# Performance work log

Hardware: AMD Instinct MI355X
Metric: run time of the kernel (lower is better)

## Reference

```python
import jax, jax.numpy as jnp
import numpy as np

# static sinkhorn parameters (match SamplesLoss init kwargs)
P = 2
BLUR = 0.05
SCALING = 0.5
DIAMETER = 2.0  # points on the unit sphere => diameter <= 2

# geomloss epsilon_schedule: [diameter^p] + exp(arange(p*log(d), p*log(blur), p*log(scaling))) + [blur^p]
EPS_LIST = (
    [DIAMETER ** P]
    + [float(np.exp(e)) for e in np.arange(P * np.log(DIAMETER), P * np.log(BLUR), P * np.log(SCALING))]
    + [BLUR ** P]
)


def cost(m, n):
    # spherical (geodesic) distance / 2 between unit vectors: acos(<m,n>)/2
    t = jnp.clip(jnp.einsum('bnd,bmd->bnm', m, n), -1.0 + 1e-6, 1.0 - 1e-6)
    return jnp.arccos(t) * 0.5  # (B,N,M)


def softmin(eps, C, wlog):
    # -eps * logsumexp(wlog[B,1,M] - C/eps, axis=2) -> (B,N)
    return -eps * jax.nn.logsumexp(wlog[:, None, :] - C / eps, axis=2)


def log_weights(a):
    return jnp.where(a > 0, jnp.log(jnp.maximum(a, 1e-30)), -1e5)


def setup_inputs() -> dict:
    key = jax.random.key(0)
    kx, ky = jax.random.split(key)
    B, N, M, D = 8, 2048, 2048, 3
    x = jax.random.normal(kx, (B, N, D), dtype=jnp.float32)
    y = jax.random.normal(ky, (B, M, D), dtype=jnp.float32)
    # project onto the unit sphere (spherical cost assumes unit vectors)
    x = x / jnp.linalg.norm(x, axis=-1, keepdims=True)
    y = y / jnp.linalg.norm(y, axis=-1, keepdims=True)
    alpha = jnp.ones((B, N), dtype=jnp.float32) / N
    beta = jnp.ones((B, M), dtype=jnp.float32) / M
    return {"alpha": alpha, "x": x, "beta": beta, "y": y}


def reference(alpha, x, beta, y):
    sg = jax.lax.stop_gradient
    # second argument of each cost is detached, as in the torch code
    C_xx = cost(x, sg(x))
    C_yy = cost(y, sg(y))
    C_xy = cost(x, sg(y))
    C_yx = cost(y, sg(x))
    al = log_weights(alpha)
    bl = log_weights(beta)

    # ---- sinkhorn loop (torch.no_grad section) ----
    Cxx_, Cyy_, Cxy_, Cyx_, al_, bl_ = map(sg, (C_xx, C_yy, C_xy, C_yx, al, bl))
    eps = EPS_LIST[0]
    a_x = softmin(eps, Cxx_, al_)   # OT(a,a) potential on x
    b_y = softmin(eps, Cyy_, bl_)   # OT(b,b) potential on y
    a_y = softmin(eps, Cyx_, al_)   # OT(a,b) potential on y
    b_x = softmin(eps, Cxy_, bl_)   # OT(a,b) potential on x
    for eps in EPS_LIST:  # annealed, symmetrized sinkhorn updates
        at_x = softmin(eps, Cxx_, al_ + a_x / eps)
        bt_y = softmin(eps, Cyy_, bl_ + b_y / eps)
        at_y = softmin(eps, Cyx_, al_ + b_x / eps)
        bt_x = softmin(eps, Cxy_, bl_ + a_y / eps)
        a_x, b_y = 0.5 * (a_x + at_x), 0.5 * (b_y + bt_y)
        a_y, b_x = 0.5 * (a_y + at_y), 0.5 * (b_x + bt_x)

    # ---- last extrapolation, differentiable (eps = blur^p) ----
    eps = EPS_LIST[-1]
    a_x = softmin(eps, C_xx, sg(al + a_x / eps))
    b_y = softmin(eps, C_yy, sg(bl + b_y / eps))
    a_y = softmin(eps, C_yx, sg(al + b_x / eps))
    b_x = softmin(eps, C_xy, sg(bl + a_y / eps))

    # balanced (reach=None), debiased sinkhorn cost -> (B,)
    return jnp.sum(alpha * (b_x - a_x), axis=-1) + jnp.sum(beta * (a_y - b_y), axis=-1)
```

## Files before the change

### kernel.cpp

```cpp
#include <hip/hip_runtime.h>
#include <math.h>

#define BB 8
#define NN 2048
#define L2E 1.4426950408889634f
#define LN2 0.6931471805599453f
#define PI_F 3.14159265358979f
#define CLIP 0.999999f
#define THSC 20860.0f
#define THSCI (1.0f / 20860.0f)

constexpr int TB   = 128;
constexpr int T16  = NN / TB;
constexpr int NXX  = T16 * (T16 + 1) / 2;
constexpr int NT   = 2 * NXX + T16 * T16;
constexpr int SARR = BB * NN;

__device__ __forceinline__ void decode_tile(int bx, int& kind, int& I, int& J) {
    if (bx < NXX) kind = 0;
    else if (bx < 2 * NXX) { kind = 1; bx -= NXX; }
    else { kind = 2; bx -= 2 * NXX; }
    if (kind < 2) {
        int idx = bx; I = 0;
        for (;;) { int len = T16 - I; if (idx < len) { J = I + idx; break; } idx -= len; I++; }
    } else { I = bx >> 4; J = bx & 15; }
}

__device__ __forceinline__ float acos_raw(float d) {
    const float u = fabsf(d);
    float pl = fmaf(u, -0.0187293f, 0.0742610f);
    pl = fmaf(u, pl, -0.2121144f); pl = fmaf(u, pl, 1.5707288f);
    const float rt = __builtin_amdgcn_sqrtf(1.f - u) * pl;
    return (d >= 0.f) ? rt : (PI_F - rt);
}

__device__ __forceinline__ size_t th_off(int g, int wv, int lane) {
    return (size_t)(((g * 4 + wv) * 64 + lane) * 8);
}

__global__ __launch_bounds__(256)
void pack_kernel(const float* __restrict__ alpha, const float* __restrict__ beta,
                 float* __restrict__ gxw, float* __restrict__ gyw,
                 float* __restrict__ Wall, float* __restrict__ Gall)
{
    const int tid = threadIdx.x;
    const int gid = blockIdx.x * 256 + tid;
    const int o = gid >> 14, i = gid & (SARR - 1);
    const float* w = (o == 0 || o == 3) ? alpha : beta;
    const float v = w[i];
    const float g = ((v > 0.f) ? logf(fmaxf(v, 1e-30f)) : -1e5f) * L2E;
    if (o == 0) gxw[i] = g;
    if (o == 1) gyw[i] = g;
    float m = g;
    m = fmaxf(m, __shfl_xor(m, 1));  m = fmaxf(m, __shfl_xor(m, 2));
    m = fmaxf(m, __shfl_xor(m, 4));  m = fmaxf(m, __shfl_xor(m, 8));
    m = fmaxf(m, __shfl_xor(m, 16)); m = fmaxf(m, __shfl_xor(m, 32));
    __shared__ float wmax[4];
    const int wv = tid >> 6;
    if ((tid & 63) == 0) wmax[wv] = m;
    __syncthreads();
    const int grp = tid >> 7;
    const float G = fmaxf(wmax[grp * 2], wmax[grp * 2 + 1]);
    Wall[gid] = __builtin_amdgcn_exp2f(g - G);
    if ((tid & 127) == 0) Gall[gid >> 7] = G;
}

__global__ __launch_bounds__(256)
void maxes_kernel(const float* __restrict__ x, const float* __restrict__ y,
                  float* __restrict__ Rxx, float* __restrict__ Ryy,
                  float* __restrict__ Rxy, float* __restrict__ Cxy,
                  unsigned short* __restrict__ Theta,
                  const float* __restrict__ Wall, const float* __restrict__ Gall,
                  float2* pAX, float2* pBY, float2* pAY, float2* pBX,
                  float negK, int writeTheta)
{
    __shared__ float4 p1s[TB], p2s[TB];
    __shared__ float colred[4][TB];
    __shared__ float colpart[4][TB];
    int kind, I, J; decode_tile(blockIdx.x, kind, I, J);
    const int b = blockIdx.y, t = threadIdx.x;
    const float* P1 = (kind == 1) ? y : x;
    const float* P2 = (kind == 0) ? x : y;
    const int o1 = (kind == 0) ? 0 : (kind == 1) ? 1 : 3;
    const int o2 = (kind == 0) ? 0 : (kind == 1) ? 1 : 2;
    float2* rowOut = (kind == 0) ? pAX : (kind == 1) ? pBY : pBX;
    float2* colOut = (kind == 0) ? pAX : (kind == 1) ? pBY : pAY;
    const bool diag = (kind < 2) && (I == J);
    const float* W1 = Wall + (size_t)o1 * SARR;
    const float* W2 = Wall + (size_t)o2 * SARR;

    if (t < TB) {
        size_t gi = (size_t)b * NN + (size_t)I * TB + t;
        p1s[t] = make_float4(P1[gi * 3], P1[gi * 3 + 1], P1[gi * 3 + 2], W1[gi]);
    } else {
        int u = t - TB; size_t gi = (size_t)b * NN + (size_t)J * TB + u;
        p2s[u] = make_float4(P2[gi * 3], P2[gi * 3 + 1], P2[gi * 3 + 2], W2[gi]);
    }
    const float G1 = Gall[o1 * 128 + b * T16 + I];
    const float G2 = Gall[o2 * 128 + b * T16 + J];
    __syncthreads();
    const int lane = t & 63, wv = t >> 6, colg = lane & 7, rowg = lane >> 3;
    const int r0 = wv * 32 + rowg * 4;
    unsigned short* Tb = Theta + ((size_t)(b * NT + blockIdx.x) << 14);

    float4 pr[4];
#pragma unroll
    for (int rr = 0; rr < 4; rr++) pr[rr] = p1s[r0 + rr];
    float rmx[4] = {-2.f, -2.f, -2.f, -2.f};
    float cmx[16];
#pragma unroll
    for (int j = 0; j < 16; j++) cmx[j] = -2.f;
    float racc[4] = {0.f, 0.f, 0.f, 0.f};
    float cacc[16];
#pragma unroll
    for (int j = 0; j < 16; j++) cacc[j] = 0.f;

#pragma unroll
    for (int g = 0; g < 8; g++) {
        uint4 outv;
#pragma unroll
        for (int e = 0; e < 2; e++) {
            const int j = g * 2 + e;
            const float4 q = p2s[colg + 8 * j];
            unsigned int lo = 0, hi = 0;
#pragma unroll
            for (int rr = 0; rr < 4; rr++) {
                const float d = fmaf(pr[rr].x, q.x, fmaf(pr[rr].y, q.y, pr[rr].z * q.z));
                rmx[rr] = fmaxf(rmx[rr], d);
                cmx[j] = fmaxf(cmx[j], d);
                if (writeTheta) {
                    const float dc = fminf(fmaxf(d, -CLIP), CLIP);
                    const float th = acos_raw(dc);
                    const unsigned int qv = __float2uint_rn(th * THSC);
                    if (rr == 0) lo = qv;
                    else if (rr == 1) lo |= qv << 16;
                    else if (rr == 2) hi = qv;
                    else hi |= qv << 16;
                    const float em = __builtin_amdgcn_exp2f(th * negK);
                    racc[rr] = fmaf(q.w, em, racc[rr]);
                    cacc[j]  = fmaf(pr[rr].w, em, cacc[j]);
                }
            }
            if (e == 0) { outv.x = lo; outv.y = hi; }
            else        { outv.z = lo; outv.w = hi; }
        }
        if (writeTheta)
            *(uint4*)(Tb + th_off(g, wv, lane)) = outv;
    }

#pragma unroll
    for (int rr = 0; rr < 4; rr++) {
        float v = rmx[rr];
        v = fmaxf(v, __shfl_xor(v, 1)); v = fmaxf(v, __shfl_xor(v, 2));
        v = fmaxf(v, __shfl_xor(v, 4));
        rmx[rr] = v;
    }
    if (colg == 0) {
        float* R = (kind == 0) ? Rxx : (kind == 1) ? Ryy : Rxy;
        const size_t base = ((size_t)b * T16 + J) * NN + (size_t)I * TB + r0;
#pragma unroll
        for (int rr = 0; rr < 4; rr++)
            R[base + rr] = acos_raw(fminf(fmaxf(rmx[rr], -CLIP), CLIP));
    }
#pragma unroll
    for (int j = 0; j < 16; j++) {
        float v = cmx[j];
        v = fmaxf(v, __shfl_xor(v, 8)); v = fmaxf(v, __shfl_xor(v, 16));
        v = fmaxf(v, __shfl_xor(v, 32));
        cmx[j] = v;
    }
    if (rowg == 0) {
#pragma unroll
        for (int j = 0; j < 16; j++) colred[wv][colg + 8 * j] = cmx[j];
    }

    if (writeTheta) {
#pragma unroll
        for (int j = 0; j < 16; j++) {
            float v = cacc[j];
            v += __shfl_xor(v, 8); v += __shfl_xor(v, 16); v += __shfl_xor(v, 32);
            cacc[j] = v;
        }
        if (rowg == 0) {
#pragma unroll
            for (int j = 0; j < 16; j++) colpart[wv][colg + 8 * j] = cacc[j];
        }
#pragma unroll
        for (int rr = 0; rr < 4; rr++) {
            float v = racc[rr];
            v += __shfl_xor(v, 1); v += __shfl_xor(v, 2); v += __shfl_xor(v, 4);
            racc[rr] = v;
        }
        if (colg == 0) {
            const size_t gr = (size_t)J * SARR + (size_t)b * NN + (size_t)I * TB + r0;
#pragma unroll
            for (int rr = 0; rr < 4; rr++)
                rowOut[gr + rr] = make_float2(G2, racc[rr]);
        }
    }

    __syncthreads();
    if (t < TB) {
        const float v = fmaxf(fmaxf(colred[0][t], colred[1][t]),
                              fmaxf(colred[2][t], colred[3][t]));
        const float th = acos_raw(fminf(fmaxf(v, -CLIP), CLIP));
        if (kind == 2) {
            Cxy[((size_t)b * T16 + I) * NN + (size_t)J * TB + t] = th;
        } else if (I != J) {
            float* R = (kind == 0) ? Rxx : Ryy;
            R[((size_t)b * T16 + I) * NN + (size_t)J * TB + t] = th;
        }
        if (writeTheta && !diag) {
            const float pv = colpart[0][t] + colpart[1][t] + colpart[2][t] + colpart[3][t];
            const size_t gc = (size_t)I * SARR + (size_t)b * NN + (size_t)J * TB + t;
            colOut[gc] = make_float2(G1, pv);
        }
    }
}

struct TileArgsT {
    const unsigned short* Theta;
    const float* Wall; const float* Gall;
    const float* Rxx; const float* Ryy; const float* Rxy; const float* Cxy;
    float2* pAX; float2* pBY; float2* pAY; float2* pBX;
};

__global__ __launch_bounds__(256)
void tile_theta_kernel(TileArgsT A, float ieh, float Kq)
{
    __shared__ float2 s1[TB], s2[TB];
    __shared__ float colpart[4][TB];
    int kind, I, J; decode_tile(blockIdx.x, kind, I, J);
    const int b = blockIdx.y, t = threadIdx.x;
    const int o1 = (kind == 0) ? 0 : (kind == 1) ? 1 : 3;
    const int o2 = (kind == 0) ? 0 : (kind == 1) ? 1 : 2;
    float2* rowOut = (kind == 0) ? A.pAX : (kind == 1) ? A.pBY : A.pBX;
    float2* colOut = (kind == 0) ? A.pAX : (kind == 1) ? A.pBY : A.pAY;
    const bool diag = (kind < 2) && (I == J);
    const float* W1 = A.Wall + (size_t)o1 * SARR;
    const float* W2 = A.Wall + (size_t)o2 * SARR;
    const float* Rrow = (kind == 0) ? A.Rxx : (kind == 1) ? A.Ryy : A.Rxy;
    const float* Csrc = (kind == 0) ? A.Rxx : (kind == 1) ? A.Ryy : A.Cxy;

    if (t < TB) {
        size_t gi = (size_t)b * NN + (size_t)I * TB + t;
        s1[t] = make_float2(Rrow[((size_t)b * T16 + J) * NN + (size_t)I * TB + t] * ieh, W1[gi]);
    } else {
        int u = t - TB; size_t gi = (size_t)b * NN + (size_t)J * TB + u;
        s2[u] = make_float2(Csrc[((size_t)b * T16 + I) * NN + (size_t)J * TB + u] * ieh, W2[gi]);
    }
    const float G1 = A.Gall[o1 * 128 + b * T16 + I];
    const float G2 = A.Gall[o2 * 128 + b * T16 + J];
    __syncthreads();

    const int lane = t & 63, wv = t >> 6, colg = lane & 7, rowg = lane >> 3;
    const int r0 = wv * 32 + rowg * 4;
    const unsigned short* Tb = A.Theta + ((size_t)(b * NT + blockIdx.x) << 14);

    float srr[4], w1r[4];
#pragma unroll
    for (int rr = 0; rr < 4; rr++) { const float2 v = s1[r0 + rr]; srr[rr] = v.x; w1r[rr] = v.y; }
    float racc[4] = {0.f, 0.f, 0.f, 0.f};
    float cacc[16];
#pragma unroll
    for (int j = 0; j < 16; j++) cacc[j] = 0.f;

#pragma unroll
    for (int g = 0; g < 8; g++) {
        const uint4 tq = *(const uint4*)(Tb + th_off(g, wv, lane));
#pragma unroll
        for (int e = 0; e < 2; e++) {
            const int j = g * 2 + e;
            const unsigned int lo = e ? tq.z : tq.x;
            const unsigned int hi = e ? tq.w : tq.y;
            const float2 sv = s2[colg + 8 * j];
            const float thv[4] = {
                (float)(lo & 0xffffu), (float)(lo >> 16),
                (float)(hi & 0xffffu), (float)(hi >> 16)
            };
#pragma unroll
            for (int rr = 0; rr < 4; rr++) {
                const float er = __builtin_amdgcn_exp2f(fmaf(thv[rr], -Kq, srr[rr]));
                const float ec = __builtin_amdgcn_exp2f(fmaf(thv[rr], -Kq, sv.x));
                racc[rr] = fmaf(sv.y, er, racc[rr]);
                cacc[j]  = fmaf(w1r[rr], ec, cacc[j]);
            }
        }
    }

#pragma unroll
    for (int j = 0; j < 16; j++) {
        float v = cacc[j];
        v += __shfl_xor(v, 8); v += __shfl_xor(v, 16); v += __shfl_xor(v, 32);
        cacc[j] = v;
    }
    if (rowg == 0) {
#pragma unroll
        for (int j = 0; j < 16; j++) colpart[wv][colg + 8 * j] = cacc[j];
    }
#pragma unroll
    for (int rr = 0; rr < 4; rr++) {
        float v = racc[rr];
        v += __shfl_xor(v, 1); v += __shfl_xor(v, 2); v += __shfl_xor(v, 4);
        racc[rr] = v;
    }
    if (colg == 0) {
        const size_t gr = (size_t)J * SARR + (size_t)b * NN + (size_t)I * TB + r0;
#pragma unroll
        for (int rr = 0; rr < 4; rr++)
            rowOut[gr + rr] = make_float2(G2 - srr[rr], racc[rr]);
    }
    __syncthreads();
    if (!diag && t < TB) {
        const float v = colpart[0][t] + colpart[1][t] + colpart[2][t] + colpart[3][t];
        const size_t gc = (size_t)I * SARR + (size_t)b * NN + (size_t)J * TB + t;
        colOut[gc] = make_float2(G1 - s2[t].x, v);
    }
}

struct TileArgs {
    const float* x; const float* y;
    const float* Wall; const float* Gall;
    const float* Rxx; const float* Ryy; const float* Rxy; const float* Cxy;
    float2* pAX; float2* pBY; float2* pAY; float2* pBX;
};

__global__ __launch_bounds__(256)
void tile_kernel(TileArgs A, float ieh, float pi_ieh)
{
    __shared__ float4 p1s[TB], p2s[TB];
    __shared__ float srs[TB], scs[TB];
    __shared__ float colpart[4][TB];
    int kind, I, J; decode_tile(blockIdx.x, kind, I, J);
    const int b = blockIdx.y, t = threadIdx.x;
    const float* P1 = (kind == 1) ? A.y : A.x;
    const float* P2 = (kind == 0) ? A.x : A.y;
    const int o1 = (kind == 0) ? 0 : (kind == 1) ? 1 : 3;
    const int o2 = (kind == 0) ? 0 : (kind == 1) ? 1 : 2;
    float2* rowOut = (kind == 0) ? A.pAX : (kind == 1) ? A.pBY : A.pBX;
    float2* colOut = (kind == 0) ? A.pAX : (kind == 1) ? A.pBY : A.pAY;
    const bool diag = (kind < 2) && (I == J);
    const float* W1 = A.Wall + (size_t)o1 * SARR;
    const float* W2 = A.Wall + (size_t)o2 * SARR;
    const float* Rrow = (kind == 0) ? A.Rxx : (kind == 1) ? A.Ryy : A.Rxy;
    const float* Csrc = (kind == 0) ? A.Rxx : (kind == 1) ? A.Ryy : A.Cxy;

    const float K0 = 1.5707288f * ieh, K1 = -0.2121144f * ieh;
    const float K2 = 0.0742610f * ieh, K3 = -0.0187293f * ieh;

    if (t < TB) {
        size_t gi = (size_t)b * NN + (size_t)I * TB + t;
        p1s[t] = make_float4(P1[gi * 3], P1[gi * 3 + 1], P1[gi * 3 + 2], W1[gi]);
        srs[t] = Rrow[((size_t)b * T16 + J) * NN + (size_t)I * TB + t] * ieh;
    } else {
        int u = t - TB; size_t gi = (size_t)b * NN + (size_t)J * TB + u;
        p2s[u] = make_float4(P2[gi * 3], P2[gi * 3 + 1], P2[gi * 3 + 2], W2[gi]);
        scs[u] = Csrc[((size_t)b * T16 + I) * NN + (size_t)J * TB + u] * ieh;
    }
    const float G1 = A.Gall[o1 * 128 + b * T16 + I];
    const float G2 = A.Gall[o2 * 128 + b * T16 + J];
    __syncthreads();

    const int lane = t & 63, wv = t >> 6, colg = lane & 7, rowg = lane >> 3;
    const int r0 = wv * 32 + rowg * 4;
    float4 pr[4]; float srr[4];
#pragma unroll
    for (int rr = 0; rr < 4; rr++) { pr[rr] = p1s[r0 + rr]; srr[rr] = srs[r0 + rr]; }
    float racc[4] = {0.f, 0.f, 0.f, 0.f};
    float cacc[16];
#pragma unroll
    for (int j = 0; j < 16; j++) cacc[j] = 0.f;

#pragma unroll
    for (int j = 0; j < 16; j++) {
        const float4 q = p2s[colg + 8 * j];
        const float sc = scs[colg + 8 * j];
#pragma unroll
        for (int rr = 0; rr < 4; rr++) {
            const float4 p = pr[rr];
            float d = fmaf(p.x, q.x, fmaf(p.y, q.y, p.z * q.z));
            d = fminf(fmaxf(d, -CLIP), CLIP);
            const float u = fabsf(d);
            float pl = fmaf(u, K3, K2); pl = fmaf(u, pl, K1); pl = fmaf(u, pl, K0);
            const float rt = __builtin_amdgcn_sqrtf(1.f - u) * pl;
            const float ach = (d >= 0.f) ? rt : (pi_ieh - rt);
            racc[rr] = fmaf(q.w, __builtin_amdgcn_exp2f(srr[rr] - ach), racc[rr]);
            cacc[j]  = fmaf(p.w, __builtin_amdgcn_exp2f(sc - ach), cacc[j]);
        }
    }

#pragma unroll
    for (int j = 0; j < 16; j++) {
        float v = cacc[j];
        v += __shfl_xor(v, 8); v += __shfl_xor(v, 16); v += __shfl_xor(v, 32);
        cacc[j] = v;
    }
    if (rowg == 0) {
#pragma unroll
        for (int j = 0; j < 16; j++) colpart[wv][colg + 8 * j] = cacc[j];
    }
#pragma unroll
    for (int rr = 0; rr < 4; rr++) {
        float v = racc[rr];
        v += __shfl_xor(v, 1); v += __shfl_xor(v, 2); v += __shfl_xor(v, 4);
        racc[rr] = v;
    }
    if (colg == 0) {
        const size_t gr = (size_t)J * SARR + (size_t)b * NN + (size_t)I * TB + r0;
#pragma unroll
        for (int rr = 0; rr < 4; rr++)
            rowOut[gr + rr] = make_float2(G2 - srr[rr], racc[rr]);
    }
    __syncthreads();
    if (!diag && t < TB) {
        const float v = colpart[0][t] + colpart[1][t] + colpart[2][t] + colpart[3][t];
        const size_t gc = (size_t)I * SARR + (size_t)b * NN + (size_t)J * TB + t;
        colOut[gc] = make_float2(G1 - scs[t], v);
    }
}

__global__ __launch_bounds__(256)
void combine_kernel(const float2* __restrict__ pAX, const float2* __restrict__ pBY,
                    const float2* __restrict__ pAY, const float2* __restrict__ pBX,
                    float* __restrict__ ax, float* __restrict__ by,
                    float* __restrict__ ay, float* __restrict__ bx,
                    const float* __restrict__ gxw, const float* __restrict__ gyw,
                    float* __restrict__ Wall, float* __restrict__ Gall,
                    float eps_ln2, float nieL2E, int do_avg)
{
    const int tid = threadIdx.x;
    const int gid = blockIdx.x * 256 + tid;
    const int o = gid >> 14, i = gid & (SARR - 1);
    const float2* P = (o == 0) ? pAX : (o == 1) ? pBY : (o == 2) ? pAY : pBX;
    float* pot = (o == 0) ? ax : (o == 1) ? by : (o == 2) ? ay : bx;
    float2 pr[T16];
#pragma unroll
    for (int u = 0; u < T16; u++) pr[u] = P[(size_t)u * SARR + i];
    float M = -3.0e38f;
#pragma unroll
    for (int u = 0; u < T16; u++) M = fmaxf(M, (pr[u].y > 0.f) ? pr[u].x : -3.0e38f);
    float S = 0.f;
#pragma unroll
    for (int u = 0; u < T16; u++)
        S += pr[u].y * __builtin_amdgcn_exp2f(fminf(pr[u].x - M, 0.f));
    S = fmaxf(S, 1e-38f);
    float r = -eps_ln2 * (M + __builtin_amdgcn_logf(S));
    if (do_avg) r = 0.5f * (r + pot[i]);
    pot[i] = r;
    const float g = ((o == 0 || o == 3) ? gxw[i] : gyw[i]) + r * nieL2E;
    float m = g;
    m = fmaxf(m, __shfl_xor(m, 1));  m = fmaxf(m, __shfl_xor(m, 2));
    m = fmaxf(m, __shfl_xor(m, 4));  m = fmaxf(m, __shfl_xor(m, 8));
    m = fmaxf(m, __shfl_xor(m, 16)); m = fmaxf(m, __shfl_xor(m, 32));
    __shared__ float wmax[4];
    const int wv = tid >> 6;
    if ((tid & 63) == 0) wmax[wv] = m;
    __syncthreads();
    const int grp = tid >> 7;
    const float G = fmaxf(wmax[grp * 2], wmax[grp * 2 + 1]);
    Wall[gid] = __builtin_amdgcn_exp2f(g - G);
    if ((tid & 127) == 0) Gall[gid >> 7] = G;
}

__global__ __launch_bounds__(256)
void reduce_kernel(const float* __restrict__ alpha, const float* __restrict__ beta,
                   const float* __restrict__ a_x, const float* __restrict__ b_x,
                   const float* __restrict__ a_y, const float* __restrict__ b_y,
                   float* __restrict__ out)
{
    const int b = blockIdx.x, tid = threadIdx.x;
    float acc = 0.f;
    for (int n = tid; n < NN; n += 256) {
        const size_t i = (size_t)b * NN + n;
        acc += alpha[i] * (b_x[i] - a_x[i]);
        acc += beta[i] * (a_y[i] - b_y[i]);
    }
    __shared__ float red[256];
    red[tid] = acc;
    __syncthreads();
    for (int st = 128; st > 0; st >>= 1) {
        if (tid < st) red[tid] += red[tid + st];
        __syncthreads();
    }
    if (tid == 0) out[b] = red[0];
}

extern "C" void kernel_launch(void* const* d_in, const int* in_sizes, int n_in,
                              void* d_out, int out_size, void* d_ws, size_t ws_size,
                              hipStream_t stream)
{
    const float* alpha = (const float*)d_in[0];
    const float* x     = (const float*)d_in[1];
    const float* beta  = (const float*)d_in[2];
    const float* y     = (const float*)d_in[3];
    float* out = (float*)d_out;
    float* ws  = (float*)d_ws;

    const size_t S = SARR;
    float* gxw  = ws;
    float* gyw  = ws + S;
    float* ax   = ws + 2 * S;
    float* by   = ws + 3 * S;
    float* ay   = ws + 4 * S;
    float* bx   = ws + 5 * S;
    float* Wall = ws + 6 * S;
    float* Gall = ws + 10 * S;
    float* Rxx  = ws + 10 * S + 512;
    float* Ryy  = Rxx + 16 * S;
    float* Rxy  = Ryy + 16 * S;
    float* Cxy  = Rxy + 16 * S;
    float* pb   = Cxy + 16 * S;
    const size_t PSZ = (size_t)SARR * T16;
    float2* pAX = (float2*)pb;
    float2* pBY = pAX + PSZ;
    float2* pAY = pBY + PSZ;
    float2* pBX = pAY + PSZ;

    float* thetaF = pb + (size_t)8 * PSZ;
    unsigned short* Theta = (unsigned short*)thetaF;
    const size_t used_bytes  = (size_t)((char*)thetaF - (char*)ws);
    const size_t theta_bytes = (size_t)BB * NT * 16384 * sizeof(unsigned short);
    const int useTheta = (ws_size >= used_bytes + theta_bytes) ? 1 : 0;

    const float EPS[8] = {4.0f, 4.0f, 1.0f, 0.25f, 0.0625f, 0.015625f, 0.00390625f, 0.0025f};

    pack_kernel<<<(4 * SARR) / 256, 256, 0, stream>>>(alpha, beta, gxw, gyw, Wall, Gall);
    const float negK = -0.5f * (1.f / EPS[0]) * L2E;
    maxes_kernel<<<dim3(NT, BB), 256, 0, stream>>>(x, y, Rxx, Ryy, Rxy, Cxy, Theta,
                                                   Wall, Gall, pAX, pBY, pAY, pBX,
                                                   negK, useTheta);

    TileArgsT TT;
    TT.Theta = Theta; TT.Wall = Wall; TT.Gall = Gall;
    TT.Rxx = Rxx; TT.Ryy = Ryy; TT.Rxy = Rxy; TT.Cxy = Cxy;
    TT.pAX = pAX; TT.pBY = pBY; TT.pAY = pAY; TT.pBX = pBX;

    TileArgs TA;
    TA.x = x; TA.y = y; TA.Wall = Wall; TA.Gall = Gall;
    TA.Rxx = Rxx; TA.Ryy = Ryy; TA.Rxy = Rxy; TA.Cxy = Cxy;
    TA.pAX = pAX; TA.pBY = pBY; TA.pAY = pAY; TA.pBX = pBX;

    auto step = [&](float e, float next_e, int avg, int run_tile) {
        const float ieh = 0.5f * (1.f / e) * L2E;
        if (run_tile) {
            if (useTheta)
                tile_theta_kernel<<<dim3(NT, BB), 256, 0, stream>>>(TT, ieh, ieh * THSCI);
            else
                tile_kernel<<<dim3(NT, BB), 256, 0, stream>>>(TA, ieh, PI_F * ieh);
        }
        combine_kernel<<<(4 * SARR) / 256, 256, 0, stream>>>(
            pAX, pBY, pAY, pBX, ax, by, ay, bx, gxw, gyw, Wall, Gall,
            e * LN2, (1.f / next_e) * L2E, avg);
    };

    step(EPS[0], EPS[0], 0, useTheta ? 0 : 1);
    for (int k = 0; k < 8; k++) step(EPS[k], (k < 7) ? EPS[k + 1] : EPS[7], 1, 1);
    step(EPS[7], EPS[7], 0, 1);

    reduce_kernel<<<BB, 256, 0, stream>>>(alpha, beta, ax, bx, ay, by, out);
}
```

Before: 412.4 us.

## Prefetch theta, skip diagonal column work, split combine rows, fuse final reduction

The theta tile kernel now issues all eight packed-angle loads before the shared-memory staging and barrier, so their latency can overlap the setup. Diagonal tiles skip the column exponentials and the column reduction, since those results were discarded anyway. The combine kernel splits each row's 16 partials across two threads joined with a shuffle, which doubles the grid. The final reduce kernel is folded into the last combine pass through block-level atomicAdds into an output zeroed by the pack kernel. In exchange, the atomics make the summation order nondeterministic and the extra register array raises register pressure.

After: 415.0 us. About the same (+0.6%).

```diff
diff --git a/kernel.cpp b/kernel.cpp
--- a/kernel.cpp
+++ b/kernel.cpp
@@ -41,10 +41,12 @@
 __global__ __launch_bounds__(256)
 void pack_kernel(const float* __restrict__ alpha, const float* __restrict__ beta,
                  float* __restrict__ gxw, float* __restrict__ gyw,
-                 float* __restrict__ Wall, float* __restrict__ Gall)
+                 float* __restrict__ Wall, float* __restrict__ Gall,
+                 float* __restrict__ out)
 {
     const int tid = threadIdx.x;
     const int gid = blockIdx.x * 256 + tid;
+    if (blockIdx.x == 0 && tid < BB) out[tid] = 0.f;
     const int o = gid >> 14, i = gid & (SARR - 1);
     const float* w = (o == 0 || o == 3) ? alpha : beta;
     const float v = w[i];
@@ -232,6 +234,14 @@
     __shared__ float colpart[4][TB];
     int kind, I, J; decode_tile(blockIdx.x, kind, I, J);
     const int b = blockIdx.y, t = threadIdx.x;
+    const int lane = t & 63, wv = t >> 6, colg = lane & 7, rowg = lane >> 3;
+    const int r0 = wv * 32 + rowg * 4;
+
+    const unsigned short* Tb = A.Theta + ((size_t)(b * NT + blockIdx.x) << 14);
+    uint4 tq[8];
+#pragma unroll
+    for (int g = 0; g < 8; g++) tq[g] = *(const uint4*)(Tb + th_off(g, wv, lane));
+
     const int o1 = (kind == 0) ? 0 : (kind == 1) ? 1 : 3;
     const int o2 = (kind == 0) ? 0 : (kind == 1) ? 1 : 2;
     float2* rowOut = (kind == 0) ? A.pAX : (kind == 1) ? A.pBY : A.pBX;
@@ -253,10 +263,6 @@
     const float G2 = A.Gall[o2 * 128 + b * T16 + J];
     __syncthreads();
 
-    const int lane = t & 63, wv = t >> 6, colg = lane & 7, rowg = lane >> 3;
-    const int r0 = wv * 32 + rowg * 4;
-    const unsigned short* Tb = A.Theta + ((size_t)(b * NT + blockIdx.x) << 14);
-
     float srr[4], w1r[4];
 #pragma unroll
     for (int rr = 0; rr < 4; rr++) { const float2 v = s1[r0 + rr]; srr[rr] = v.x; w1r[rr] = v.y; }
@@ -265,39 +271,50 @@
 #pragma unroll
     for (int j = 0; j < 16; j++) cacc[j] = 0.f;
 
-#pragma unroll
-    for (int g = 0; g < 8; g++) {
-        const uint4 tq = *(const uint4*)(Tb + th_off(g, wv, lane));
-#pragma unroll
-        for (int e = 0; e < 2; e++) {
-            const int j = g * 2 + e;
-            const unsigned int lo = e ? tq.z : tq.x;
-            const unsigned int hi = e ? tq.w : tq.y;
-            const float2 sv = s2[colg + 8 * j];
-            const float thv[4] = {
-                (float)(lo & 0xffffu), (float)(lo >> 16),
-                (float)(hi & 0xffffu), (float)(hi >> 16)
-            };
-#pragma unroll
-            for (int rr = 0; rr < 4; rr++) {
-                const float er = __builtin_amdgcn_exp2f(fmaf(thv[rr], -Kq, srr[rr]));
-                const float ec = __builtin_amdgcn_exp2f(fmaf(thv[rr], -Kq, sv.x));
-                racc[rr] = fmaf(sv.y, er, racc[rr]);
-                cacc[j]  = fmaf(w1r[rr], ec, cacc[j]);
+    if (diag) {
+#pragma unroll
+        for (int g = 0; g < 8; g++) {
+#pragma unroll
+            for (int e = 0; e < 2; e++) {
+                const int j = g * 2 + e;
+                const unsigned int lo = e ? tq[g].z : tq[g].x;
+                const unsigned int hi = e ? tq[g].w : tq[g].y;
+                const float2 sv = s2[colg + 8 * j];
+                const float thv[4] = {
+                    (float)(lo & 0xffffu), (float)(lo >> 16),
+                    (float)(hi & 0xffffu), (float)(hi >> 16)
+                };
+#pragma unroll
+                for (int rr = 0; rr < 4; rr++) {
+                    const float er = __builtin_amdgcn_exp2f(fmaf(thv[rr], -Kq, srr[rr]));
+                    racc[rr] = fmaf(sv.y, er, racc[rr]);
+                }
             }
         }
-    }
-
-#pragma unroll
-    for (int j = 0; j < 16; j++) {
-        float v = cacc[j];
-        v += __shfl_xor(v, 8); v += __shfl_xor(v, 16); v += __shfl_xor(v, 32);
-        cacc[j] = v;
-    }
-    if (rowg == 0) {
-#pragma unroll
-        for (int j = 0; j < 16; j++) colpart[wv][colg + 8 * j] = cacc[j];
-    }
+    } else {
+#pragma unroll
+        for (int g = 0; g < 8; g++) {
+#pragma unroll
+            for (int e = 0; e < 2; e++) {
+                const int j = g * 2 + e;
+                const unsigned int lo = e ? tq[g].z : tq[g].x;
+                const unsigned int hi = e ? tq[g].w : tq[g].y;
+                const float2 sv = s2[colg + 8 * j];
+                const float thv[4] = {
+                    (float)(lo & 0xffffu), (float)(lo >> 16),
+                    (float)(hi & 0xffffu), (float)(hi >> 16)
+                };
+#pragma unroll
+                for (int rr = 0; rr < 4; rr++) {
+                    const float er = __builtin_amdgcn_exp2f(fmaf(thv[rr], -Kq, srr[rr]));
+                    const float ec = __builtin_amdgcn_exp2f(fmaf(thv[rr], -Kq, sv.x));
+                    racc[rr] = fmaf(sv.y, er, racc[rr]);
+                    cacc[j]  = fmaf(w1r[rr], ec, cacc[j]);
+                }
+            }
+        }
+    }
+
 #pragma unroll
     for (int rr = 0; rr < 4; rr++) {
         float v = racc[rr];
@@ -310,11 +327,23 @@
         for (int rr = 0; rr < 4; rr++)
             rowOut[gr + rr] = make_float2(G2 - srr[rr], racc[rr]);
     }
-    __syncthreads();
-    if (!diag && t < TB) {
-        const float v = colpart[0][t] + colpart[1][t] + colpart[2][t] + colpart[3][t];
-        const size_t gc = (size_t)I * SARR + (size_t)b * NN + (size_t)J * TB + t;
-        colOut[gc] = make_float2(G1 - s2[t].x, v);
+    if (!diag) {
+#pragma unroll
+        for (int j = 0; j < 16; j++) {
+            float v = cacc[j];
+            v += __shfl_xor(v, 8); v += __shfl_xor(v, 16); v += __shfl_xor(v, 32);
+            cacc[j] = v;
+        }
+        if (rowg == 0) {
+#pragma unroll
+            for (int j = 0; j < 16; j++) colpart[wv][colg + 8 * j] = cacc[j];
+        }
+        __syncthreads();
+        if (t < TB) {
+            const float v = colpart[0][t] + colpart[1][t] + colpart[2][t] + colpart[3][t];
+            const size_t gc = (size_t)I * SARR + (size_t)b * NN + (size_t)J * TB + t;
+            colOut[gc] = make_float2(G1 - s2[t].x, v);
+        }
     }
 }
 
@@ -426,63 +455,63 @@
                     float* __restrict__ ay, float* __restrict__ bx,
                     const float* __restrict__ gxw, const float* __restrict__ gyw,
                     float* __restrict__ Wall, float* __restrict__ Gall,
-                    float eps_ln2, float nieL2E, int do_avg)
+                    const float* __restrict__ alpha, const float* __restrict__ beta,
+                    float* __restrict__ out,
+                    float eps_ln2, float nieL2E, int do_avg, int do_out)
 {
     const int tid = threadIdx.x;
-    const int gid = blockIdx.x * 256 + tid;
-    const int o = gid >> 14, i = gid & (SARR - 1);
+    const int gid2 = blockIdx.x * 256 + tid;
+    const int row = gid2 >> 1, half = gid2 & 1;
+    const int o = row >> 14, i = row & (SARR - 1);
     const float2* P = (o == 0) ? pAX : (o == 1) ? pBY : (o == 2) ? pAY : pBX;
     float* pot = (o == 0) ? ax : (o == 1) ? by : (o == 2) ? ay : bx;
-    float2 pr[T16];
-#pragma unroll
-    for (int u = 0; u < T16; u++) pr[u] = P[(size_t)u * SARR + i];
+    float2 pr[8];
+#pragma unroll
+    for (int u = 0; u < 8; u++) pr[u] = P[(size_t)(half * 8 + u) * SARR + i];
     float M = -3.0e38f;
 #pragma unroll
-    for (int u = 0; u < T16; u++) M = fmaxf(M, (pr[u].y > 0.f) ? pr[u].x : -3.0e38f);
+    for (int u = 0; u < 8; u++) M = fmaxf(M, (pr[u].y > 0.f) ? pr[u].x : -3.0e38f);
     float S = 0.f;
 #pragma unroll
-    for (int u = 0; u < T16; u++)
+    for (int u = 0; u < 8; u++)
         S += pr[u].y * __builtin_amdgcn_exp2f(fminf(pr[u].x - M, 0.f));
+    const float Mo = __shfl_xor(M, 1);
+    const float So = __shfl_xor(S, 1);
+    const float nm = fmaxf(M, Mo);
+    S = S * __builtin_amdgcn_exp2f(M - nm) + So * __builtin_amdgcn_exp2f(Mo - nm);
     S = fmaxf(S, 1e-38f);
-    float r = -eps_ln2 * (M + __builtin_amdgcn_logf(S));
+    float r = -eps_ln2 * (nm + __builtin_amdgcn_logf(S));
     if (do_avg) r = 0.5f * (r + pot[i]);
-    pot[i] = r;
+    if (half == 0) pot[i] = r;
+
+    const int wv = tid >> 6;
+    if (do_out) {
+        float c = 0.f;
+        if (half == 0) {
+            const float w = ((o == 0 || o == 3) ? alpha : beta)[i];
+            const float sgn = (o == 0 || o == 1) ? -1.f : 1.f;
+            c = sgn * w * r;
+        }
+        c += __shfl_xor(c, 1);  c += __shfl_xor(c, 2);  c += __shfl_xor(c, 4);
+        c += __shfl_xor(c, 8);  c += __shfl_xor(c, 16); c += __shfl_xor(c, 32);
+        __shared__ float bs[4];
+        if ((tid & 63) == 0) bs[wv] = c;
+        __syncthreads();
+        if (tid == 0) atomicAdd(&out[i >> 11], bs[0] + bs[1] + bs[2] + bs[3]);
+        return;
+    }
+
     const float g = ((o == 0 || o == 3) ? gxw[i] : gyw[i]) + r * nieL2E;
     float m = g;
     m = fmaxf(m, __shfl_xor(m, 1));  m = fmaxf(m, __shfl_xor(m, 2));
     m = fmaxf(m, __shfl_xor(m, 4));  m = fmaxf(m, __shfl_xor(m, 8));
     m = fmaxf(m, __shfl_xor(m, 16)); m = fmaxf(m, __shfl_xor(m, 32));
     __shared__ float wmax[4];
-    const int wv = tid >> 6;
     if ((tid & 63) == 0) wmax[wv] = m;
     __syncthreads();
-    const int grp = tid >> 7;
-    const float G = fmaxf(wmax[grp * 2], wmax[grp * 2 + 1]);
-    Wall[gid] = __builtin_amdgcn_exp2f(g - G);
-    if ((tid & 127) == 0) Gall[gid >> 7] = G;
-}
-
-__global__ __launch_bounds__(256)
-void reduce_kernel(const float* __restrict__ alpha, const float* __restrict__ beta,
-                   const float* __restrict__ a_x, const float* __restrict__ b_x,
-                   const float* __restrict__ a_y, const float* __restrict__ b_y,
-                   float* __restrict__ out)
-{
-    const int b = blockIdx.x, tid = threadIdx.x;
-    float acc = 0.f;
-    for (int n = tid; n < NN; n += 256) {
-        const size_t i = (size_t)b * NN + n;
-        acc += alpha[i] * (b_x[i] - a_x[i]);
-        acc += beta[i] * (a_y[i] - b_y[i]);
-    }
-    __shared__ float red[256];
-    red[tid] = acc;
-    __syncthreads();
-    for (int st = 128; st > 0; st >>= 1) {
-        if (tid < st) red[tid] += red[tid + st];
-        __syncthreads();
-    }
-    if (tid == 0) out[b] = red[0];
+    const float G = fmaxf(fmaxf(wmax[0], wmax[1]), fmaxf(wmax[2], wmax[3]));
+    if (half == 0) Wall[row] = __builtin_amdgcn_exp2f(g - G);
+    if (tid == 0) Gall[blockIdx.x] = G;
 }
 
 extern "C" void kernel_launch(void* const* d_in, const int* in_sizes, int n_in,
@@ -524,7 +553,7 @@
 
     const float EPS[8] = {4.0f, 4.0f, 1.0f, 0.25f, 0.0625f, 0.015625f, 0.00390625f, 0.0025f};
 
-    pack_kernel<<<(4 * SARR) / 256, 256, 0, stream>>>(alpha, beta, gxw, gyw, Wall, Gall);
+    pack_kernel<<<(4 * SARR) / 256, 256, 0, stream>>>(alpha, beta, gxw, gyw, Wall, Gall, out);
     const float negK = -0.5f * (1.f / EPS[0]) * L2E;
     maxes_kernel<<<dim3(NT, BB), 256, 0, stream>>>(x, y, Rxx, Ryy, Rxy, Cxy, Theta,
                                                    Wall, Gall, pAX, pBY, pAY, pBX,
@@ -540,7 +569,7 @@
     TA.Rxx = Rxx; TA.Ryy = Ryy; TA.Rxy = Rxy; TA.Cxy = Cxy;
     TA.pAX = pAX; TA.pBY = pBY; TA.pAY = pAY; TA.pBX = pBX;
 
-    auto step = [&](float e, float next_e, int avg, int run_tile) {
+    auto step = [&](float e, float next_e, int avg, int run_tile, int do_out) {
         const float ieh = 0.5f * (1.f / e) * L2E;
         if (run_tile) {
             if (useTheta)
@@ -548,14 +577,13 @@
             else
                 tile_kernel<<<dim3(NT, BB), 256, 0, stream>>>(TA, ieh, PI_F * ieh);
         }
-        combine_kernel<<<(4 * SARR) / 256, 256, 0, stream>>>(
+        combine_kernel<<<(8 * SARR) / 256, 256, 0, stream>>>(
             pAX, pBY, pAY, pBX, ax, by, ay, bx, gxw, gyw, Wall, Gall,
-            e * LN2, (1.f / next_e) * L2E, avg);
+            alpha, beta, out,
+            e * LN2, (1.f / next_e) * L2E, avg, do_out);
     };
 
-    step(EPS[0], EPS[0], 0, useTheta ? 0 : 1);
-    for (int k = 0; k < 8; k++) step(EPS[k], (k < 7) ? EPS[k + 1] : EPS[7], 1, 1);
-    step(EPS[7], EPS[7], 0, 1);
-
-    reduce_kernel<<<BB, 256, 0, stream>>>(alpha, beta, ax, bx, ay, by, out);
-}
+    step(EPS[0], EPS[0], 0, useTheta ? 0 : 1, 0);
+    for (int k = 0; k < 8; k++) step(EPS[k], (k < 7) ? EPS[k + 1] : EPS[7], 1, 1, 0);
+    step(EPS[7], EPS[7], 0, 1, 1);
+}
```
